# Kernel tuning notes

Hardware: AMD Instinct MI355X
Metric: run time of the kernel (lower is better)

Reference implementation:

```python
import jax, jax.numpy as jnp
import numpy as np

N, E, H, ED, TD = 10000, 320000, 128, 64, 32

def _lin(x, w, b):
    return x @ w + b

def _ln(x, g, b, eps=1e-5):
    m = jnp.mean(x, axis=-1, keepdims=True)
    v = jnp.var(x, axis=-1, keepdims=True)
    return (x - m) * jax.lax.rsqrt(v + eps) * g + b

def _mlp(x, w1, b1, g, bt, w2, b2):
    y = jax.nn.silu(_ln(_lin(x, w1, b1), g, bt))
    return _lin(y, w2, b2)

def setup_inputs() -> dict:
    key = jax.random.key(0)
    ks = jax.random.split(key, 32)
    s = 0.02
    nrm = lambda k, shp: jax.random.normal(k, shp, jnp.float32) * s
    d = {}
    d['h'] = jax.random.normal(ks[0], (N, H), jnp.float32)
    d['edge_attr'] = jax.random.normal(ks[1], (E, ED), jnp.float32)
    d['edge_time_emb'] = jax.random.normal(ks[2], (E, TD), jnp.float32)
    d['edge_index'] = jax.random.randint(ks[3], (2, E), 0, N)
    # edge_emb + edge_norm
    d['w_ee'] = nrm(ks[4], (ED + TD, ED)); d['b_ee'] = jnp.zeros((ED,), jnp.float32)
    d['g_en'] = jnp.ones((ED + TD,), jnp.float32); d['bt_en'] = jnp.zeros((ED + TD,), jnp.float32)
    # node_linear / bond_linear
    d['w_nl'] = nrm(ks[5], (H, H)); d['b_nl'] = jnp.zeros((H,), jnp.float32)
    d['w_bl'] = nrm(ks[6], (ED, H)); d['b_bl'] = jnp.zeros((H,), jnp.float32)
    # bond_linear_left/right, node_linear_left/right
    d['w_bll'] = nrm(ks[7], (ED, H)); d['b_bll'] = jnp.zeros((H,), jnp.float32)
    d['w_blr'] = nrm(ks[8], (ED, H)); d['b_blr'] = jnp.zeros((H,), jnp.float32)
    d['w_nll'] = nrm(ks[9], (H, H)); d['b_nll'] = jnp.zeros((H,), jnp.float32)
    d['w_nlr'] = nrm(ks[10], (H, H)); d['b_nlr'] = jnp.zeros((H,), jnp.float32)
    # left / right MLPs: Linear(2H,H), LayerNorm(H), SiLU, Linear(H,H)
    d['mlpl_w1'] = nrm(ks[11], (2 * H, H)); d['mlpl_b1'] = jnp.zeros((H,), jnp.float32)
    d['mlpl_g'] = jnp.ones((H,), jnp.float32); d['mlpl_bt'] = jnp.zeros((H,), jnp.float32)
    d['mlpl_w2'] = nrm(ks[12], (H, H)); d['mlpl_b2'] = jnp.zeros((H,), jnp.float32)
    d['mlpr_w1'] = nrm(ks[13], (2 * H, H)); d['mlpr_b1'] = jnp.zeros((H,), jnp.float32)
    d['mlpr_g'] = jnp.ones((H,), jnp.float32); d['mlpr_bt'] = jnp.zeros((H,), jnp.float32)
    d['mlpr_w2'] = nrm(ks[14], (H, H)); d['mlpr_b2'] = jnp.zeros((H,), jnp.float32)
    # layer_norm(3H) + bond_out: Linear(3H,H), SiLU, Linear(H,ED)
    d['g_ln'] = jnp.ones((3 * H,), jnp.float32); d['bt_ln'] = jnp.zeros((3 * H,), jnp.float32)
    d['w_o1'] = nrm(ks[15], (3 * H, H)); d['b_o1'] = jnp.zeros((H,), jnp.float32)
    d['w_o2'] = nrm(ks[16], (H, ED)); d['b_o2'] = jnp.zeros((ED,), jnp.float32)
    return d

def reference(h, edge_attr, edge_time_emb, edge_index,
              w_ee, b_ee, g_en, bt_en, w_nl, b_nl, w_bl, b_bl,
              w_bll, b_bll, w_blr, b_blr, w_nll, b_nll, w_nlr, b_nlr,
              mlpl_w1, mlpl_b1, mlpl_g, mlpl_bt, mlpl_w2, mlpl_b2,
              mlpr_w1, mlpr_b1, mlpr_g, mlpr_bt, mlpr_w2, mlpr_b2,
              g_ln, bt_ln, w_o1, b_o1, w_o2, b_o2):
    src, dst = edge_index[0], edge_index[1]
    n = h.shape[0]
    # edge_attr = edge_emb(edge_norm(cat([edge_attr, edge_time_emb])))
    ea = _lin(_ln(jnp.concatenate([edge_attr, edge_time_emb], axis=-1), g_en, bt_en), w_ee, b_ee)
    # node linears applied per-node then gathered (same math as gather-then-linear)
    x_i = _lin(h, w_nll, b_nll)[src]            # [E, H]
    x_j = _lin(h, w_nlr, b_nlr)[dst]            # [E, H]
    edge_i = _lin(ea, w_bll, b_bll)             # [E, H]
    edge_j = _lin(ea, w_blr, b_blr)             # [E, H]
    inter_i = _mlp(jnp.concatenate([edge_i, x_i], axis=-1), mlpl_w1, mlpl_b1, mlpl_g, mlpl_bt, mlpl_w2, mlpl_b2)
    inter_j = _mlp(jnp.concatenate([edge_j, x_j], axis=-1), mlpr_w1, mlpr_b1, mlpr_g, mlpr_bt, mlpr_w2, mlpr_b2)
    # scatter_sum to nodes, then regather on the same index
    inter_i = jax.ops.segment_sum(inter_i, src, num_segments=n)[src]
    inter_j = jax.ops.segment_sum(inter_j, dst, num_segments=n)[dst]
    h_node = _lin(h, w_nl, b_nl)
    h_bond = jnp.concatenate([inter_i + inter_j, h_node[src] + h_node[dst], _lin(ea, w_bl, b_bl)], axis=-1)  # [E, 3H]
    h_bond = _ln(h_bond, g_ln, bt_ln)
    out = _lin(jax.nn.silu(_lin(h_bond, w_o1, b_o1)), w_o2, b_o2)  # [E, ED]
    return out
```

## Files before the change

kernel.cpp:

```cpp
#include <hip/hip_runtime.h>
#include <math.h>


using u16 = unsigned short;
using u32 = unsigned int;
typedef __attribute__((ext_vector_type(8))) short  short8;
typedef __attribute__((ext_vector_type(4))) float  f32x4;
typedef __attribute__((ext_vector_type(4))) u32    uint4v;
typedef __attribute__((ext_vector_type(2))) u32    uint2v;

constexpr int NN = 10000;
constexpr int EE = 320000;
constexpr int MAXDEG = 96;

__device__ __forceinline__ float b2f(u16 v) {
  return __builtin_bit_cast(float, (u32)v << 16);
}
__device__ __forceinline__ float b2f_lo(u32 v) {
  return __builtin_bit_cast(float, v << 16);
}
__device__ __forceinline__ float b2f_hi(u32 v) {
  return __builtin_bit_cast(float, v & 0xffff0000u);
}
__device__ __forceinline__ u32 cvtpk(float lo, float hi) {
  u32 r;
  asm("v_cvt_pk_bf16_f32 %0, %1, %2" : "=v"(r) : "v"(lo), "v"(hi));
  return r;
}
__device__ __forceinline__ u16 f2b(float f) {
  return (u16)cvtpk(f, f);
}
__device__ __forceinline__ uint2v pack4(f32x4 v) {
  uint2v r;
  r.x = cvtpk(v[0], v[1]);
  r.y = cvtpk(v[2], v[3]);
  return r;
}
__device__ __forceinline__ u32 addpk(u32 a, u32 b) {
  return cvtpk(b2f_lo(a) + b2f_lo(b), b2f_hi(a) + b2f_hi(b));
}
__device__ __forceinline__ float silu_f(float v) {
  return v * __builtin_amdgcn_rcpf(1.f + __expf(-v));
}

struct Params {
  const void* h; const void* edge_attr; const void* te;
  const int* eidx;
  const int* flag;
  const u16 *b_ee, *g_en, *bt_en;
  const u16 *b_nl, *b_bl, *b_bll, *b_blr, *b_nll, *b_nlr;
  const u16 *l_b1, *l_g, *l_bt, *l_b2;
  const u16 *r_b1, *r_g, *r_bt, *r_b2;
  const u16 *g_ln, *bt_ln, *b_o1, *b_o2;
  const u16 *w_eeT, *w_blT, *w_bllT, *w_blrT, *w_nlT, *w_nllT, *w_nlrT;
  const u16 *l_w1T, *l_w2T, *r_w1T, *r_w2T, *o1T, *o2T;
  u16 *a_nll, *a_nlr, *h_node, *ea_ws;
  u32 *cnt0, *cnt1, *elist0, *elist1;
  u16 *accb_i, *accb_j;
  float *accf_i, *accf_j;
  u16 *inter0, *inter1;
  int amode;
  void *out;
};

__global__ __launch_bounds__(256) void k_sniff(const u16* p, int* flag)
{
  __shared__ int c;
  if (threadIdx.x == 0) c = 0;
  __syncthreads();
  u16 v = p[threadIdx.x * 2];
  int e = (v >> 7) & 0xff;
  if (e >= 100 && e <= 140) atomicAdd(&c, 1);
  __syncthreads();
  if (threadIdx.x == 0) *flag = (c >= 200) ? 1 : 0;
}

template<int K, int CT, int RT>
__device__ __forceinline__ void wave_gemm(const u16* A, int SA,
                                          const u16* __restrict__ BT,
                                          f32x4 (&acc)[RT][CT], int n0)
{
  const int lane = threadIdx.x & 63;
  const int quad = lane >> 4, l16 = lane & 15;
#pragma unroll
  for (int kt = 0; kt < K / 32; ++kt) {
    const int k0 = kt * 32 + quad * 8;
    short8 b[CT];
#pragma unroll
    for (int c = 0; c < CT; ++c)
      b[c] = *(const short8*)(BT + (size_t)(n0 + c * 16 + l16) * K + k0);
#pragma unroll
    for (int rt = 0; rt < RT; ++rt) {
      short8 av = *(const short8*)(A + (rt * 16 + l16) * SA + k0);
#pragma unroll
      for (int c = 0; c < CT; ++c)
        acc[rt][c] = __builtin_amdgcn_mfma_f32_16x16x32_bf16(av, b[c], acc[rt][c], 0, 0, 0);
    }
  }
}

template<int CT, int RT, bool SILU>
__device__ __forceinline__ void epi_lds(f32x4 (&acc)[RT][CT], u16* O, int SO,
                                        int outc0, const u16* __restrict__ bias,
                                        int biasc0)
{
  const int lane = threadIdx.x & 63;
  const int quad = lane >> 4, l16 = lane & 15;
#pragma unroll
  for (int c = 0; c < CT; ++c) {
    float bv = b2f(bias[biasc0 + c * 16 + l16]);
#pragma unroll
    for (int rt = 0; rt < RT; ++rt) {
#pragma unroll
      for (int r = 0; r < 4; ++r) {
        float v = acc[rt][c][r] + bv;
        if (SILU) v = silu_f(v);
        O[(rt * 16 + quad * 4 + r) * SO + outc0 + c * 16 + l16] = f2b(v);
      }
    }
  }
}

template<int D, int ROWS, bool SILU>
__device__ __forceinline__ void ln_rows(u16* buf, int S,
                                        const u16* __restrict__ g,
                                        const u16* __restrict__ bt, float* red)
{
  constexpr int P = 256 / ROWS;
  constexpr int C = D / P;
  constexpr int NV = C / 8;
  const int t = threadIdx.x;
  const int row = t / P, p = t % P;
  u16* r = buf + row * S + p * C;
  uint4v vv[NV];
  float s = 0.f, ss = 0.f;
#pragma unroll
  for (int n = 0; n < NV; ++n) {
    vv[n] = *(const uint4v*)(r + n * 8);
#pragma unroll
    for (int q = 0; q < 4; ++q) {
      float lo = b2f_lo(vv[n][q]), hi = b2f_hi(vv[n][q]);
      s += lo + hi;
      ss += lo * lo + hi * hi;
    }
  }
  red[row * 2 * P + p] = s;
  red[row * 2 * P + P + p] = ss;
  __syncthreads();
  float S1 = 0.f, S2 = 0.f;
#pragma unroll
  for (int q = 0; q < P / 4; ++q) {
    f32x4 x = *(const f32x4*)&red[row * 2 * P + q * 4];
    f32x4 y = *(const f32x4*)&red[row * 2 * P + P + q * 4];
    S1 += x[0] + x[1] + x[2] + x[3];
    S2 += y[0] + y[1] + y[2] + y[3];
  }
  const float mean = S1 / (float)D;
  const float var  = S2 / (float)D - mean * mean;
  const float rstd = rsqrtf(var + 1e-5f);
#pragma unroll
  for (int n = 0; n < NV; ++n) {
    uint4v gv = *(const uint4v*)(g + p * C + n * 8);
    uint4v bv = *(const uint4v*)(bt + p * C + n * 8);
    uint4v ov;
#pragma unroll
    for (int q = 0; q < 4; ++q) {
      float lo = (b2f_lo(vv[n][q]) - mean) * rstd * b2f_lo(gv[q]) + b2f_lo(bv[q]);
      float hi = (b2f_hi(vv[n][q]) - mean) * rstd * b2f_hi(gv[q]) + b2f_hi(bv[q]);
      if (SILU) { lo = silu_f(lo); hi = silu_f(hi); }
      ov[q] = cvtpk(lo, hi);
    }
    *(uint4v*)(r + n * 8) = ov;
  }
  __syncthreads();
}

struct TDesc { const void* s; u16* d; int K; int N; };
struct TArgs { TDesc t[34]; const int* flag; };

__global__ __launch_bounds__(256) void k_transpose(TArgs a)
{
  const int flag = *a.flag;
  TDesc dsc = a.t[blockIdx.y];
  const int total = dsc.K * dsc.N;
  for (int i = blockIdx.x * 256 + threadIdx.x; i < total; i += gridDim.x * 256) {
    int n = i / dsc.K;
    int k = i - n * dsc.K;
    size_t si = (size_t)k * dsc.N + n;
    dsc.d[i] = flag ? ((const u16*)dsc.s)[si] : f2b(((const float*)dsc.s)[si]);
  }
}

__global__ __launch_bounds__(256) void k_hist(const int* eidx, u32* cnt0,
                                              u32* elist0, u32* cnt1, u32* elist1)
{
  int e = blockIdx.x * 256 + threadIdx.x;
  if (e >= EE) return;
  int n0 = eidx[e];
  u32 p0 = atomicAdd(&cnt0[n0], 1u);
  if (p0 < MAXDEG) elist0[(size_t)n0 * MAXDEG + p0] = (u32)e;
  int n1 = eidx[EE + e];
  u32 p1 = atomicAdd(&cnt1[n1], 1u);
  if (p1 < MAXDEG) elist1[(size_t)n1 * MAXDEG + p1] = (u32)e;
}

__global__ __launch_bounds__(256) void k_node(Params a)
{
  __shared__ __align__(16) u16 hs[64 * 136];
  const int tid = threadIdx.x, w = tid >> 6;
  const int n0 = blockIdx.x * 64;
  const int flag = *a.flag;
  if (flag) {
    for (int c = tid; c < 1024; c += 256) {
      int row = c >> 4, cc = c & 15;
      int node = n0 + row;
      uint4v v = {};
      if (node < NN) v = *(const uint4v*)((const u16*)a.h + (size_t)node * 128 + cc * 8);
      *(uint4v*)&hs[row * 136 + cc * 8] = v;
    }
  } else {
    for (int c = tid; c < 2048; c += 256) {
      int row = c >> 5, cc = c & 31;
      int node = n0 + row;
      uint2v pk = {};
      if (node < NN) {
        f32x4 fv = *(const f32x4*)((const float*)a.h + (size_t)node * 128 + cc * 4);
        pk = pack4(fv);
      }
      *(uint2v*)&hs[row * 136 + cc * 4] = pk;
    }
  }
  __syncthreads();
  const u16* wT[3] = { a.w_nllT, a.w_nlrT, a.w_nlT };
  const u16* bs[3] = { a.b_nll, a.b_nlr, a.b_nl };
  u16* os[3] = { a.a_nll, a.a_nlr, a.h_node };
  const int lane = tid & 63, quad = lane >> 4, l16 = lane & 15;
#pragma unroll 1
  for (int m = 0; m < 3; ++m) {
    f32x4 acc[4][2] = {};
    wave_gemm<128, 2, 4>(hs, 136, wT[m], acc, w * 32);
#pragma unroll
    for (int c = 0; c < 2; ++c) {
      int col = w * 32 + c * 16 + l16;
      float bv = b2f(bs[m][col]);
#pragma unroll
      for (int rt = 0; rt < 4; ++rt) {
#pragma unroll
        for (int r = 0; r < 4; ++r) {
          int node = n0 + rt * 16 + quad * 4 + r;
          if (node < NN) os[m][(size_t)node * 128 + col] = f2b(acc[rt][c][r] + bv);
        }
      }
    }
  }
}

__global__ __launch_bounds__(256) void k_ea(Params a)
{
  __shared__ __align__(16) u16 u[64 * 104];
  __shared__ __align__(16) u16 eas[64 * 72];
  __shared__ float red[512];
  const int tid = threadIdx.x, w = tid >> 6;
  const int e0 = blockIdx.x * 64;
  const int flag = *a.flag;
  if (flag) {
    for (int c = tid; c < 512; c += 256) {
      int row = c >> 3, cc = c & 7;
      *(uint4v*)&u[row * 104 + cc * 8] =
          *(const uint4v*)((const u16*)a.edge_attr + (size_t)(e0 + row) * 64 + cc * 8);
    }
    {
      int row = tid >> 2, cc = tid & 3;
      *(uint4v*)&u[row * 104 + 64 + cc * 8] =
          *(const uint4v*)((const u16*)a.te + (size_t)(e0 + row) * 32 + cc * 8);
    }
  } else {
    for (int c = tid; c < 1024; c += 256) {
      int row = c >> 4, cc = c & 15;
      f32x4 fv = *(const f32x4*)((const float*)a.edge_attr + (size_t)(e0 + row) * 64 + cc * 4);
      *(uint2v*)&u[row * 104 + cc * 4] = pack4(fv);
    }
    for (int c = tid; c < 512; c += 256) {
      int row = c >> 3, cc = c & 7;
      f32x4 fv = *(const f32x4*)((const float*)a.te + (size_t)(e0 + row) * 32 + cc * 4);
      *(uint2v*)&u[row * 104 + 64 + cc * 4] = pack4(fv);
    }
  }
  __syncthreads();
  ln_rows<96, 64, false>(u, 104, a.g_en, a.bt_en, red);
  {
    f32x4 acc[4][1] = {};
    wave_gemm<96, 1, 4>(u, 104, a.w_eeT, acc, w * 16);
    epi_lds<1, 4, false>(acc, eas, 72, w * 16, a.b_ee, w * 16);
  }
  __syncthreads();
  for (int c = tid; c < 512; c += 256) {
    int row = c >> 3, cc = c & 7;
    *(uint4v*)(a.ea_ws + (size_t)(e0 + row) * 64 + cc * 8) =
        *(const uint4v*)&eas[row * 72 + cc * 8];
  }
}

template<bool ATOMIC>
__global__ __launch_bounds__(256) void k_mlp(
    const u16* __restrict__ ea_ws, const int* __restrict__ eidx_side,
    const u16* __restrict__ an, const u16* __restrict__ wbT,
    const u16* __restrict__ bb, const u16* __restrict__ w1T,
    const u16* __restrict__ b1, const u16* __restrict__ gg,
    const u16* __restrict__ bt, const u16* __restrict__ w2T,
    const u16* __restrict__ b2, u16* __restrict__ inter,
    float* __restrict__ accf)
{
  __shared__ __align__(16) u16 u[64 * 264];
  __shared__ __align__(16) u16 eas[64 * 72];
  __shared__ float red[512];
  __shared__ int sidx[64];
  const int tid = threadIdx.x, w = tid >> 6;
  const int e0 = blockIdx.x * 64;
  const int lane = tid & 63, quad = lane >> 4, l16 = lane & 15;

  if (tid < 64) sidx[tid] = eidx_side[e0 + tid];
  for (int c = tid; c < 512; c += 256) {
    int row = c >> 3, cc = c & 7;
    *(uint4v*)&eas[row * 72 + cc * 8] =
        *(const uint4v*)(ea_ws + (size_t)(e0 + row) * 64 + cc * 8);
  }
  __syncthreads();
  for (int c = tid; c < 1024; c += 256) {
    int row = c >> 4, cc = c & 15;
    *(uint4v*)&u[row * 264 + 128 + cc * 8] =
        *(const uint4v*)(an + (size_t)sidx[row] * 128 + cc * 8);
  }
  {
    f32x4 acc[4][2] = {};
    wave_gemm<64, 2, 4>(eas, 72, wbT, acc, w * 32);
    epi_lds<2, 4, false>(acc, u, 264, w * 32, bb, w * 32);
  }
  __syncthreads();
  {
    f32x4 acc[4][2] = {};
    wave_gemm<256, 2, 4>(u, 264, w1T, acc, w * 32);
    __syncthreads();
    epi_lds<2, 4, false>(acc, u, 264, w * 32, b1, w * 32);
  }
  __syncthreads();
  ln_rows<128, 64, true>(u, 264, gg, bt, red);
  {
    f32x4 acc[4][2] = {};
    wave_gemm<128, 2, 4>(u, 264, w2T, acc, w * 32);
    if (ATOMIC) {
#pragma unroll
      for (int c = 0; c < 2; ++c) {
        int col = w * 32 + c * 16 + l16;
        float bias = b2f(b2[col]);
#pragma unroll
        for (int rt = 0; rt < 4; ++rt)
#pragma unroll
          for (int r = 0; r < 4; ++r) {
            int row = rt * 16 + quad * 4 + r;
            unsafeAtomicAdd(accf + (size_t)sidx[row] * 128 + col,
                            acc[rt][c][r] + bias);
          }
      }
    } else {
      epi_lds<2, 4, false>(acc, u, 264, 128 + w * 32, b2, w * 32);
      __syncthreads();
      for (int c = tid; c < 1024; c += 256) {
        int row = c >> 4, cc = c & 15;
        *(uint4v*)(inter + (size_t)(e0 + row) * 128 + cc * 8) =
            *(const uint4v*)&u[row * 264 + 128 + cc * 8];
      }
    }
  }
}

__global__ __launch_bounds__(256) void k_nodesum(const u16* __restrict__ inter,
                                                 const u32* __restrict__ cnt,
                                                 const u32* __restrict__ elist,
                                                 u16* __restrict__ accb)
{
  const int wv = (blockIdx.x * 256 + threadIdx.x) >> 6;
  const int lane = threadIdx.x & 63;
  if (wv >= NN) return;
  u32 deg = cnt[wv];
  if (deg > MAXDEG) deg = MAXDEG;
  const u32* el = elist + (size_t)wv * MAXDEG;
  float s0 = 0.f, s1 = 0.f;
  u32 d = 0;
  for (; d + 4 <= deg; d += 4) {
    uint4v ev = *(const uint4v*)(el + d);
    u32 v0 = *(const u32*)(inter + (size_t)ev[0] * 128 + lane * 2);
    u32 v1 = *(const u32*)(inter + (size_t)ev[1] * 128 + lane * 2);
    u32 v2 = *(const u32*)(inter + (size_t)ev[2] * 128 + lane * 2);
    u32 v3 = *(const u32*)(inter + (size_t)ev[3] * 128 + lane * 2);
    s0 += b2f_lo(v0) + b2f_lo(v1) + b2f_lo(v2) + b2f_lo(v3);
    s1 += b2f_hi(v0) + b2f_hi(v1) + b2f_hi(v2) + b2f_hi(v3);
  }
  for (; d < deg; ++d) {
    u32 e = el[d];
    u32 v = *(const u32*)(inter + (size_t)e * 128 + lane * 2);
    s0 += b2f_lo(v);
    s1 += b2f_hi(v);
  }
  *(u32*)(accb + (size_t)wv * 128 + lane * 2) = cvtpk(s0, s1);
}

__global__ __launch_bounds__(256) void k_stage2(Params a)
{
  __shared__ __align__(16) u16 bond[32 * 392];
  __shared__ __align__(16) u16 eas[32 * 72];
  __shared__ float red[512];
  __shared__ int sidx[2][32];
  const int tid = threadIdx.x, w = tid >> 6;
  const int e0 = blockIdx.x * 32;
  const int flag = *a.flag;
  const int lane = tid & 63, quad = lane >> 4, l16 = lane & 15;

  if (tid < 64) {
    int side = tid >> 5, i = tid & 31;
    sidx[side][i] = a.eidx[(size_t)side * EE + e0 + i];
  }
  {
    int row = tid >> 3, cc = tid & 7;
    *(uint4v*)&eas[row * 72 + cc * 8] =
        *(const uint4v*)(a.ea_ws + (size_t)(e0 + row) * 64 + cc * 8);
  }
  __syncthreads();
  if (a.amode) {
    for (int c = tid; c < 1024; c += 256) {
      int row = c >> 5, cc = c & 31;
      uint2v vi = *(const uint2v*)(a.accb_i + (size_t)sidx[0][row] * 128 + cc * 4);
      uint2v vj = *(const uint2v*)(a.accb_j + (size_t)sidx[1][row] * 128 + cc * 4);
      uint2v ov;
      ov.x = addpk(vi.x, vj.x);
      ov.y = addpk(vi.y, vj.y);
      *(uint2v*)&bond[row * 392 + cc * 4] = ov;
    }
  } else {
    for (int c = tid; c < 1024; c += 256) {
      int row = c >> 5, cc = c & 31;
      f32x4 vi = *(const f32x4*)(a.accf_i + (size_t)sidx[0][row] * 128 + cc * 4);
      f32x4 vj = *(const f32x4*)(a.accf_j + (size_t)sidx[1][row] * 128 + cc * 4);
      f32x4 sm = vi + vj;
      *(uint2v*)&bond[row * 392 + cc * 4] = pack4(sm);
    }
  }
  for (int c = tid; c < 512; c += 256) {
    int row = c >> 4, cc = c & 15;
    uint4v hs = *(const uint4v*)(a.h_node + (size_t)sidx[0][row] * 128 + cc * 8);
    uint4v hd = *(const uint4v*)(a.h_node + (size_t)sidx[1][row] * 128 + cc * 8);
    uint4v ov;
#pragma unroll
    for (int q = 0; q < 4; ++q) ov[q] = addpk(hs[q], hd[q]);
    *(uint4v*)&bond[row * 392 + 128 + cc * 8] = ov;
  }
  {
    f32x4 acc[2][2] = {};
    wave_gemm<64, 2, 2>(eas, 72, a.w_blT, acc, w * 32);
    epi_lds<2, 2, false>(acc, bond, 392, 256 + w * 32, a.b_bl, w * 32);
  }
  __syncthreads();
  ln_rows<384, 32, false>(bond, 392, a.g_ln, a.bt_ln, red);
  {
    f32x4 acc[2][2] = {};
    wave_gemm<384, 2, 2>(bond, 392, a.o1T, acc, w * 32);
    __syncthreads();
    epi_lds<2, 2, true>(acc, bond, 392, w * 32, a.b_o1, w * 32);
  }
  __syncthreads();
  {
    f32x4 acc[2][1] = {};
    wave_gemm<128, 1, 2>(bond, 392, a.o2T, acc, w * 16);
    if (flag) {
      epi_lds<1, 2, false>(acc, bond, 392, 128 + w * 16, a.b_o2, w * 16);
      __syncthreads();
      for (int c = tid; c < 256; c += 256) {
        int row = c >> 3, cc = c & 7;
        *(uint4v*)((u16*)a.out + (size_t)(e0 + row) * 64 + cc * 8) =
            *(const uint4v*)&bond[row * 392 + 128 + cc * 8];
      }
    } else {
      float bvv = b2f(a.b_o2[w * 16 + l16]);
#pragma unroll
      for (int rt = 0; rt < 2; ++rt)
#pragma unroll
        for (int r = 0; r < 4; ++r) {
          int row = rt * 16 + quad * 4 + r;
          ((float*)((char*)bond + (size_t)row * 784 + 272))[w * 16 + l16] =
              acc[rt][0][r] + bvv;
        }
      __syncthreads();
      for (int c = tid; c < 512; c += 256) {
        int row = c >> 4, cc = c & 15;
        f32x4 v = *(const f32x4*)((char*)bond + (size_t)row * 784 + 272 + cc * 16);
        *(f32x4*)((float*)a.out + (size_t)(e0 + row) * 64 + cc * 4) = v;
      }
    }
  }
}

extern "C" void kernel_launch(void* const* d_in, const int* in_sizes, int n_in,
                              void* d_out, int out_size, void* d_ws, size_t ws_size,
                              hipStream_t stream)
{
  char* ws = (char*)d_ws;

  const size_t O_EET  = 0;
  const size_t O_BLT  = 12288;
  const size_t O_BLLT = O_BLT  + 16384;
  const size_t O_BLRT = O_BLLT + 16384;
  const size_t O_NLT  = O_BLRT + 16384;
  const size_t O_NLLT = O_NLT  + 32768;
  const size_t O_NLRT = O_NLLT + 32768;
  const size_t O_LW1T = O_NLRT + 32768;
  const size_t O_LW2T = O_LW1T + 65536;
  const size_t O_RW1T = O_LW2T + 32768;
  const size_t O_RW2T = O_RW1T + 65536;
  const size_t O_O1T  = O_RW2T + 32768;
  const size_t O_O2T  = O_O1T  + 98304;
  const size_t PRM    = O_O2T  + 16384;
  const size_t FLAG   = PRM + 6016;
  const size_t A_NLL  = PRM + 6144;
  const size_t A_NLR  = A_NLL + 2560000;
  const size_t H_NODE = A_NLR + 2560000;
  const size_t EA     = H_NODE + 2560000;
  const size_t TAIL   = EA + 40960000;
  const size_t ACCF_I = TAIL;
  const size_t ACCF_J = TAIL + 5120000;
  const size_t NEED_ATOM = TAIL + 10240000;
  const size_t CNT0   = TAIL;
  const size_t CNT1   = TAIL + 40960;
  const size_t EL0    = TAIL + 81920;
  const size_t EL1    = EL0 + 3840000;
  const size_t ACCB_I = EL1 + 3840000;
  const size_t ACCB_J = ACCB_I + 2560000;
  const size_t INTER0 = ACCB_J + 2560000;
  const size_t NEED_CSR = INTER0 + 81920000;
  if (ws_size < NEED_ATOM) return;
  const int amode = (ws_size >= NEED_CSR) ? 1 : 0;

  const size_t pOff[21] = { 0, 128, 320, 512, 768, 1024, 1280, 1536, 1792,
                            2048, 2304, 2560, 2816, 3072, 3328, 3584, 3840,
                            4096, 4864, 5632, 5888 };
  const int   pIdx[21] = { 5, 6, 7, 9, 11, 13, 15, 17, 19,
                           21, 22, 23, 25, 27, 28, 29, 31,
                           32, 33, 35, 37 };
  const int   pLen[21] = { 64, 96, 96, 128, 128, 128, 128, 128, 128,
                           128, 128, 128, 128, 128, 128, 128, 128,
                           384, 384, 128, 64 };
  auto P = [&](int slot) { return (const u16*)(ws + PRM + pOff[slot]); };

  Params a;
  a.h = d_in[0]; a.edge_attr = d_in[1]; a.te = d_in[2];
  a.eidx = (const int*)d_in[3];
  a.flag = (const int*)(ws + FLAG);
  a.b_ee = P(0); a.g_en = P(1); a.bt_en = P(2);
  a.b_nl = P(3); a.b_bl = P(4); a.b_bll = P(5); a.b_blr = P(6);
  a.b_nll = P(7); a.b_nlr = P(8);
  a.l_b1 = P(9); a.l_g = P(10); a.l_bt = P(11); a.l_b2 = P(12);
  a.r_b1 = P(13); a.r_g = P(14); a.r_bt = P(15); a.r_b2 = P(16);
  a.g_ln = P(17); a.bt_ln = P(18); a.b_o1 = P(19); a.b_o2 = P(20);
  a.w_eeT = (const u16*)(ws + O_EET);   a.w_blT  = (const u16*)(ws + O_BLT);
  a.w_bllT = (const u16*)(ws + O_BLLT); a.w_blrT = (const u16*)(ws + O_BLRT);
  a.w_nlT = (const u16*)(ws + O_NLT);   a.w_nllT = (const u16*)(ws + O_NLLT);
  a.w_nlrT = (const u16*)(ws + O_NLRT);
  a.l_w1T = (const u16*)(ws + O_LW1T);  a.l_w2T = (const u16*)(ws + O_LW2T);
  a.r_w1T = (const u16*)(ws + O_RW1T);  a.r_w2T = (const u16*)(ws + O_RW2T);
  a.o1T = (const u16*)(ws + O_O1T);     a.o2T = (const u16*)(ws + O_O2T);
  a.a_nll = (u16*)(ws + A_NLL); a.a_nlr = (u16*)(ws + A_NLR);
  a.h_node = (u16*)(ws + H_NODE); a.ea_ws = (u16*)(ws + EA);
  a.cnt0 = (u32*)(ws + CNT0); a.cnt1 = (u32*)(ws + CNT1);
  a.elist0 = (u32*)(ws + EL0); a.elist1 = (u32*)(ws + EL1);
  a.accb_i = (u16*)(ws + ACCB_I); a.accb_j = (u16*)(ws + ACCB_J);
  a.accf_i = (float*)(ws + ACCF_I); a.accf_j = (float*)(ws + ACCF_J);
  a.inter0 = (u16*)(ws + INTER0); a.inter1 = (u16*)(ws + INTER0);
  a.amode = amode;
  a.out = d_out;

  TArgs ta;
  ta.flag = (const int*)(ws + FLAG);
  ta.t[0]  = { d_in[4],  (u16*)(ws + O_EET),  96, 64 };
  ta.t[1]  = { d_in[10], (u16*)(ws + O_BLT),  64, 128 };
  ta.t[2]  = { d_in[12], (u16*)(ws + O_BLLT), 64, 128 };
  ta.t[3]  = { d_in[14], (u16*)(ws + O_BLRT), 64, 128 };
  ta.t[4]  = { d_in[8],  (u16*)(ws + O_NLT),  128, 128 };
  ta.t[5]  = { d_in[16], (u16*)(ws + O_NLLT), 128, 128 };
  ta.t[6]  = { d_in[18], (u16*)(ws + O_NLRT), 128, 128 };
  ta.t[7]  = { d_in[20], (u16*)(ws + O_LW1T), 256, 128 };
  ta.t[8]  = { d_in[24], (u16*)(ws + O_LW2T), 128, 128 };
  ta.t[9]  = { d_in[26], (u16*)(ws + O_RW1T), 256, 128 };
  ta.t[10] = { d_in[30], (u16*)(ws + O_RW2T), 128, 128 };
  ta.t[11] = { d_in[34], (u16*)(ws + O_O1T),  384, 128 };
  ta.t[12] = { d_in[36], (u16*)(ws + O_O2T),  128, 64 };
  for (int s = 0; s < 21; ++s)
    ta.t[13 + s] = { d_in[pIdx[s]], (u16*)(ws + PRM + pOff[s]), 1, pLen[s] };

  k_sniff<<<1, 256, 0, stream>>>((const u16*)d_in[1], (int*)(ws + FLAG));
  if (amode) hipMemsetAsync(ws + CNT0, 0, 81920, stream);
  else       hipMemsetAsync(ws + ACCF_I, 0, 10240000, stream);
  k_transpose<<<dim3(16, 34), 256, 0, stream>>>(ta);
  if (amode)
    k_hist<<<(EE + 255) / 256, 256, 0, stream>>>(a.eidx, a.cnt0, a.elist0, a.cnt1, a.elist1);
  k_node<<<(NN + 63) / 64, 256, 0, stream>>>(a);
  k_ea<<<EE / 64, 256, 0, stream>>>(a);

  if (amode) {
    k_mlp<false><<<EE / 64, 256, 0, stream>>>(a.ea_ws, a.eidx, a.a_nll, a.w_bllT,
        a.b_bll, a.l_w1T, a.l_b1, a.l_g, a.l_bt, a.l_w2T, a.l_b2, a.inter0, nullptr);
    k_nodesum<<<(NN * 64 + 255) / 256, 256, 0, stream>>>(a.inter0, a.cnt0, a.elist0, a.accb_i);
    k_mlp<false><<<EE / 64, 256, 0, stream>>>(a.ea_ws, a.eidx + EE, a.a_nlr, a.w_blrT,
        a.b_blr, a.r_w1T, a.r_b1, a.r_g, a.r_bt, a.r_w2T, a.r_b2, a.inter1, nullptr);
    k_nodesum<<<(NN * 64 + 255) / 256, 256, 0, stream>>>(a.inter1, a.cnt1, a.elist1, a.accb_j);
  } else {
    k_mlp<true><<<EE / 64, 256, 0, stream>>>(a.ea_ws, a.eidx, a.a_nll, a.w_bllT,
        a.b_bll, a.l_w1T, a.l_b1, a.l_g, a.l_bt, a.l_w2T, a.l_b2, nullptr, a.accf_i);
    k_mlp<true><<<EE / 64, 256, 0, stream>>>(a.ea_ws, a.eidx + EE, a.a_nlr, a.w_blrT,
        a.b_blr, a.r_w1T, a.r_b1, a.r_g, a.r_bt, a.r_w2T, a.r_b2, nullptr, a.accf_j);
  }
  k_stage2<<<EE / 32, 256, 0, stream>>>(a);
}
```

Baseline: 745.2 us.

## Software-pipeline MFMA operand loads and read edge features directly from global

wave_gemm now double-buffers its A and B operand fragments, issuing loads for the next k-step before the MFMAs of the current one so load latency overlaps compute. k_mlp and k_stage2 no longer stage edge features in LDS and instead feed the GEMM straight from the global ea_ws buffer, which frees LDS and drops a sync-dependent copy. Both kernels get a launch-bounds occupancy hint of 4 blocks per CU, and the bf16 accumulator gather in stage2 uses 16-byte vector loads. The double buffering and the occupancy hint raise register pressure and may cause spills, and the unstaged global A loads are strided rather than coalesced.

```diff
diff --git a/kernel.cpp b/kernel.cpp
--- a/kernel.cpp
+++ b/kernel.cpp
@@ -82,19 +82,36 @@
 {
   const int lane = threadIdx.x & 63;
   const int quad = lane >> 4, l16 = lane & 15;
-#pragma unroll
-  for (int kt = 0; kt < K / 32; ++kt) {
-    const int k0 = kt * 32 + quad * 8;
-    short8 b[CT];
-#pragma unroll
-    for (int c = 0; c < CT; ++c)
-      b[c] = *(const short8*)(BT + (size_t)(n0 + c * 16 + l16) * K + k0);
-#pragma unroll
-    for (int rt = 0; rt < RT; ++rt) {
-      short8 av = *(const short8*)(A + (rt * 16 + l16) * SA + k0);
+  constexpr int NKT = K / 32;
+  short8 b[CT], bn[CT], a[RT], an[RT];
+  const int k0 = quad * 8;
+#pragma unroll
+  for (int c = 0; c < CT; ++c)
+    b[c] = *(const short8*)(BT + (size_t)(n0 + c * 16 + l16) * K + k0);
+#pragma unroll
+  for (int rt = 0; rt < RT; ++rt)
+    a[rt] = *(const short8*)(A + (rt * 16 + l16) * SA + k0);
+#pragma unroll
+  for (int kt = 0; kt < NKT; ++kt) {
+    if (kt + 1 < NKT) {
+      const int k1 = (kt + 1) * 32 + quad * 8;
 #pragma unroll
       for (int c = 0; c < CT; ++c)
-        acc[rt][c] = __builtin_amdgcn_mfma_f32_16x16x32_bf16(av, b[c], acc[rt][c], 0, 0, 0);
+        bn[c] = *(const short8*)(BT + (size_t)(n0 + c * 16 + l16) * K + k1);
+#pragma unroll
+      for (int rt = 0; rt < RT; ++rt)
+        an[rt] = *(const short8*)(A + (rt * 16 + l16) * SA + k1);
+    }
+#pragma unroll
+    for (int rt = 0; rt < RT; ++rt)
+#pragma unroll
+      for (int c = 0; c < CT; ++c)
+        acc[rt][c] = __builtin_amdgcn_mfma_f32_16x16x32_bf16(a[rt], b[c], acc[rt][c], 0, 0, 0);
+    if (kt + 1 < NKT) {
+#pragma unroll
+      for (int c = 0; c < CT; ++c) b[c] = bn[c];
+#pragma unroll
+      for (int rt = 0; rt < RT; ++rt) a[rt] = an[rt];
     }
   }
 }
@@ -302,7 +319,7 @@
 }
 
 template<bool ATOMIC>
-__global__ __launch_bounds__(256) void k_mlp(
+__global__ __launch_bounds__(256, 4) void k_mlp(
     const u16* __restrict__ ea_ws, const int* __restrict__ eidx_side,
     const u16* __restrict__ an, const u16* __restrict__ wbT,
     const u16* __restrict__ bb, const u16* __restrict__ w1T,
@@ -312,7 +329,6 @@
     float* __restrict__ accf)
 {
   __shared__ __align__(16) u16 u[64 * 264];
-  __shared__ __align__(16) u16 eas[64 * 72];
   __shared__ float red[512];
   __shared__ int sidx[64];
   const int tid = threadIdx.x, w = tid >> 6;
@@ -320,11 +336,6 @@
   const int lane = tid & 63, quad = lane >> 4, l16 = lane & 15;
 
   if (tid < 64) sidx[tid] = eidx_side[e0 + tid];
-  for (int c = tid; c < 512; c += 256) {
-    int row = c >> 3, cc = c & 7;
-    *(uint4v*)&eas[row * 72 + cc * 8] =
-        *(const uint4v*)(ea_ws + (size_t)(e0 + row) * 64 + cc * 8);
-  }
   __syncthreads();
   for (int c = tid; c < 1024; c += 256) {
     int row = c >> 4, cc = c & 15;
@@ -333,7 +344,7 @@
   }
   {
     f32x4 acc[4][2] = {};
-    wave_gemm<64, 2, 4>(eas, 72, wbT, acc, w * 32);
+    wave_gemm<64, 2, 4>(ea_ws + (size_t)e0 * 64, 64, wbT, acc, w * 32);
     epi_lds<2, 4, false>(acc, u, 264, w * 32, bb, w * 32);
   }
   __syncthreads();
@@ -405,10 +416,9 @@
   *(u32*)(accb + (size_t)wv * 128 + lane * 2) = cvtpk(s0, s1);
 }
 
-__global__ __launch_bounds__(256) void k_stage2(Params a)
+__global__ __launch_bounds__(256, 4) void k_stage2(Params a)
 {
   __shared__ __align__(16) u16 bond[32 * 392];
-  __shared__ __align__(16) u16 eas[32 * 72];
   __shared__ float red[512];
   __shared__ int sidx[2][32];
   const int tid = threadIdx.x, w = tid >> 6;
@@ -420,21 +430,16 @@
     int side = tid >> 5, i = tid & 31;
     sidx[side][i] = a.eidx[(size_t)side * EE + e0 + i];
   }
-  {
-    int row = tid >> 3, cc = tid & 7;
-    *(uint4v*)&eas[row * 72 + cc * 8] =
-        *(const uint4v*)(a.ea_ws + (size_t)(e0 + row) * 64 + cc * 8);
-  }
   __syncthreads();
   if (a.amode) {
-    for (int c = tid; c < 1024; c += 256) {
-      int row = c >> 5, cc = c & 31;
-      uint2v vi = *(const uint2v*)(a.accb_i + (size_t)sidx[0][row] * 128 + cc * 4);
-      uint2v vj = *(const uint2v*)(a.accb_j + (size_t)sidx[1][row] * 128 + cc * 4);
-      uint2v ov;
-      ov.x = addpk(vi.x, vj.x);
-      ov.y = addpk(vi.y, vj.y);
-      *(uint2v*)&bond[row * 392 + cc * 4] = ov;
+    for (int c = tid; c < 512; c += 256) {
+      int row = c >> 4, cc = c & 15;
+      uint4v vi = *(const uint4v*)(a.accb_i + (size_t)sidx[0][row] * 128 + cc * 8);
+      uint4v vj = *(const uint4v*)(a.accb_j + (size_t)sidx[1][row] * 128 + cc * 8);
+      uint4v ov;
+#pragma unroll
+      for (int q = 0; q < 4; ++q) ov[q] = addpk(vi[q], vj[q]);
+      *(uint4v*)&bond[row * 392 + cc * 8] = ov;
     }
   } else {
     for (int c = tid; c < 1024; c += 256) {
@@ -456,7 +461,7 @@
   }
   {
     f32x4 acc[2][2] = {};
-    wave_gemm<64, 2, 2>(eas, 72, a.w_blT, acc, w * 32);
+    wave_gemm<64, 2, 2>(a.ea_ws + (size_t)e0 * 64, 64, a.w_blT, acc, w * 32);
     epi_lds<2, 2, false>(acc, bond, 392, 256 + w * 32, a.b_bl, w * 32);
   }
   __syncthreads();
```

Result: no change. 753.9 us (+1.2%).
